# Optimization experiments

Measured on AMD Instinct MI355X. Metric: run time of the kernel, lower is better.

The kernel has to match this reference:

```python
import jax, jax.numpy as jnp
import numpy as np

N_NODES = 100000
N_EDGES = 2000000
N_GRAPHS = 2000
IN_DIM = 7
EDGE_DIM = 4
HID = 32
N_CLASSES = 2
NEG_SLOPE = 0.2
BN_EPS = 1e-5


def setup_inputs() -> dict:
    key = jax.random.key(0)
    ks = jax.random.split(key, 16)
    x = jax.random.normal(ks[0], (N_NODES, IN_DIM), dtype=jnp.float32)
    edge_index = jax.random.randint(ks[1], (2, N_EDGES), 0, N_NODES, dtype=jnp.int64)
    batch = jnp.sort(jax.random.randint(ks[2], (N_NODES,), 0, N_GRAPHS, dtype=jnp.int64))
    edge_attr = jax.random.normal(ks[3], (N_EDGES, EDGE_DIM), dtype=jnp.float32)
    s = 0.1
    W0 = jax.random.normal(ks[4], (IN_DIM, HID), dtype=jnp.float32) * s
    W12 = jax.random.normal(ks[5], (2, HID, HID), dtype=jnp.float32) * s
    att_src = jax.random.normal(ks[6], (3, HID), dtype=jnp.float32) * s
    att_dst = jax.random.normal(ks[7], (3, HID), dtype=jnp.float32) * s
    lin_edge = jax.random.normal(ks[8], (3, EDGE_DIM, HID), dtype=jnp.float32) * s
    att_edge = jax.random.normal(ks[9], (3, HID), dtype=jnp.float32) * s
    bias = jnp.zeros((3, HID), dtype=jnp.float32)
    bn_gamma = jnp.ones((3, HID), dtype=jnp.float32)
    bn_beta = jnp.zeros((3, HID), dtype=jnp.float32)
    fc_W = jax.random.normal(ks[10], (HID, N_CLASSES), dtype=jnp.float32) * s
    fc_b = jnp.zeros((N_CLASSES,), dtype=jnp.float32)
    return dict(x=x, edge_index=edge_index, batch=batch, edge_attr=edge_attr,
                W0=W0, W12=W12, att_src=att_src, att_dst=att_dst,
                lin_edge=lin_edge, att_edge=att_edge, bias=bias,
                bn_gamma=bn_gamma, bn_beta=bn_beta, fc_W=fc_W, fc_b=fc_b)


def gat_layer(x, src, dst, edge_attr, W, a_src, a_dst, We, a_edge, b):
    # PyG GATConv, heads=1, add_self_loops=False: edge_attr conditions attention only.
    N = x.shape[0]
    h = x @ W                                   # [N, H]
    e = edge_attr @ We                          # [E, H]
    score = ((h * a_src).sum(-1)[src]
             + (h * a_dst).sum(-1)[dst]
             + (e * a_edge).sum(-1))            # [E]
    score = jax.nn.leaky_relu(score, NEG_SLOPE)
    m = jax.ops.segment_max(score, dst, num_segments=N)
    w = jnp.exp(score - m[dst])
    denom = jax.ops.segment_sum(w, dst, num_segments=N)
    alpha = w / (denom[dst] + 1e-16)            # segment softmax over incoming edges
    out = jax.ops.segment_sum(h[src] * alpha[:, None], dst, num_segments=N)
    return out + b


def batchnorm(x, gamma, beta):
    mu = x.mean(axis=0)
    var = ((x - mu) ** 2).mean(axis=0)          # biased var, as torch BN normalization
    return (x - mu) * jax.lax.rsqrt(var + BN_EPS) * gamma + beta


def reference(x, edge_index, batch, edge_attr, W0, W12, att_src, att_dst,
              lin_edge, att_edge, bias, bn_gamma, bn_beta, fc_W, fc_b):
    src, dst = edge_index[0], edge_index[1]
    Ws = [W0, W12[0], W12[1]]
    h = x
    for l in range(3):
        h = gat_layer(h, src, dst, edge_attr, Ws[l], att_src[l], att_dst[l],
                      lin_edge[l], att_edge[l], bias[l])
        h = batchnorm(h, bn_gamma[l], bn_beta[l])
        h = jax.nn.relu(h)
    node_embs = h
    graph_emb = jax.ops.segment_sum(node_embs, batch, num_segments=N_GRAPHS)
    out = graph_emb @ fc_W + fc_b
    return (out, node_embs, graph_emb)
```

## Files before the change

kernel.cpp:

```cpp
#include <hip/hip_runtime.h>
#include <hip/hip_bf16.h>
#include <math.h>

#define N_NODES   100000
#define N_EDGES   2000000
#define N_GRAPHS  2000
#define IN_DIM    7
#define EDGE_DIM  4
#define HID       32
#define N_CLASSES 2
#define NEG_SLOPE 0.2f
#define BN_EPS    1e-5f
#define SCAN_B    1024

__device__ __forceinline__ unsigned bfbits(float f) {
    unsigned u = __float_as_uint(f);
    return (u + 0x7FFFu + ((u >> 16) & 1u)) >> 16;
}

__global__ void k_ce_all(const float* __restrict__ lin_edge, const float* __restrict__ att_edge,
                         float* __restrict__ ce3, float* __restrict__ gsum3,
                         float* __restrict__ gsq3) {
    int t = threadIdx.x;
    if (t < 12) {
        int l = t >> 2, d = t & 3;
        float s = 0.f;
        for (int k = 0; k < HID; ++k)
            s += lin_edge[(size_t)l * EDGE_DIM * HID + d * HID + k] * att_edge[l * HID + k];
        ce3[t] = s;
    }
    if (t < 3 * HID) { gsum3[t] = 0.f; gsq3[t] = 0.f; }
}

__global__ void k_hist(const int* __restrict__ dst, int* __restrict__ deg) {
    int e = blockIdx.x * blockDim.x + threadIdx.x;
    if (e < N_EDGES) atomicAdd(deg + dst[e], 1);
}

__global__ void k_scan1(const int* __restrict__ deg, int* __restrict__ offs,
                        int* __restrict__ bsum) {
    __shared__ int wsum[16];
    int t = threadIdx.x, lane = t & 63, w = t >> 6;
    int i = blockIdx.x * SCAN_B + t;
    int v = (i < N_NODES) ? deg[i] : 0;
    int x = v;
#pragma unroll
    for (int o = 1; o < 64; o <<= 1) { int y = __shfl_up(x, o, 64); if (lane >= o) x += y; }
    if (lane == 63) wsum[w] = x;
    __syncthreads();
    if (t < 16) {
        int s = wsum[t];
#pragma unroll
        for (int o = 1; o < 16; o <<= 1) { int y = __shfl_up(s, o, 16); if (t >= o) s += y; }
        wsum[t] = s;
    }
    __syncthreads();
    int excl = (w ? wsum[w - 1] : 0) + x - v;
    if (i < N_NODES) offs[i] = excl;
    if (t == 0) bsum[blockIdx.x] = wsum[15];
}

__global__ void k_scan2(int* __restrict__ bsum, int nb) {
    __shared__ int w0;
    int t = threadIdx.x, lane = t & 63, w = t >> 6;
    int v = (t < nb) ? bsum[t] : 0;
    int x = v;
#pragma unroll
    for (int o = 1; o < 64; o <<= 1) { int y = __shfl_up(x, o, 64); if (lane >= o) x += y; }
    if (w == 0 && lane == 63) w0 = x;
    __syncthreads();
    int excl = x - v + (w ? w0 : 0);
    if (t < nb) bsum[t] = excl;
}

__global__ void k_scan3(int* __restrict__ offs, const int* __restrict__ bsum,
                        int* __restrict__ cursor) {
    int i = blockIdx.x * SCAN_B + threadIdx.x;
    if (i < N_NODES) {
        int o = offs[i] + bsum[blockIdx.x];
        offs[i] = o;
        cursor[i] = o;
    }
}

__global__ void k_scatter(const int* __restrict__ src, const int* __restrict__ dst,
                          const float4* __restrict__ eattr, const float* __restrict__ ce3,
                          int* __restrict__ cursor, int4* __restrict__ pack) {
    int e = blockIdx.x * blockDim.x + threadIdx.x;
    if (e >= N_EDGES) return;
    float4 ea = eattr[e];
    float e0 = ea.x * ce3[0] + ea.y * ce3[1] + ea.z * ce3[2] + ea.w * ce3[3];
    float e1 = ea.x * ce3[4] + ea.y * ce3[5] + ea.z * ce3[6] + ea.w * ce3[7];
    float e2 = ea.x * ce3[8] + ea.y * ce3[9] + ea.z * ce3[10] + ea.w * ce3[11];
    int d = dst[e];
    int pos = atomicAdd(cursor + d, 1);
    pack[pos] = make_int4(src[e],
                          (int)(bfbits(e0) | (bfbits(e1) << 16)),
                          (int)bfbits(e2), 0);
}

template <int INDIM, bool BN>
__global__ void k_linear(const float* __restrict__ in, const float* __restrict__ W,
                         const float* __restrict__ a_src, const float* __restrict__ a_dst,
                         const float* __restrict__ gsum, const float* __restrict__ gsq,
                         const float* __restrict__ gamma, const float* __restrict__ beta,
                         __hip_bfloat16* __restrict__ h, float* __restrict__ asrc,
                         float* __restrict__ adst) {
    __shared__ float Ws[INDIM * HID];
    for (int i = threadIdx.x; i < INDIM * HID; i += blockDim.x) Ws[i] = W[i];
    __syncthreads();
    int g = threadIdx.x >> 5, k = threadIdx.x & 31;
    int n = blockIdx.x * 8 + g;
    if (n >= N_NODES) return;
    float xv;
    if (BN) {
        const float invN = 1.f / (float)N_NODES;
        float mu = gsum[k] * invN;
        float var = gsq[k] * invN - mu * mu;
        var = fmaxf(var, 0.f);
        float scl = rsqrtf(var + BN_EPS) * gamma[k];
        float v = (in[(size_t)n * INDIM + k] - mu) * scl + beta[k];
        xv = fmaxf(v, 0.f);
    } else {
        xv = (k < INDIM) ? in[(size_t)n * INDIM + k] : 0.f;
    }
    float acc = 0.f;
#pragma unroll
    for (int d = 0; d < INDIM; ++d) acc += __shfl(xv, d, 32) * Ws[d * HID + k];
    h[(size_t)n * HID + k] = __float2bfloat16(acc);
    float vs = acc * a_src[k];
    float vd = acc * a_dst[k];
#pragma unroll
    for (int m = 16; m > 0; m >>= 1) {
        vs += __shfl_xor(vs, m, 32);
        vd += __shfl_xor(vd, m, 32);
    }
    if (k == 0) { asrc[n] = vs; adst[n] = vd; }
}

template <int L>
__global__ void k_aggr(const int4* __restrict__ pack, const int* __restrict__ offs,
                       const int* __restrict__ endp, const __hip_bfloat16* __restrict__ hb,
                       const float* __restrict__ asrc, const float* __restrict__ adst,
                       const float* __restrict__ bias, float* __restrict__ out,
                       float* __restrict__ gsum, float* __restrict__ gsq) {
    __shared__ float ssum[HID], ssq[HID];
    if (threadIdx.x < HID) { ssum[threadIdx.x] = 0.f; ssq[threadIdx.x] = 0.f; }
    __syncthreads();
    int g = threadIdx.x >> 5;
    int lane = threadIdx.x & 31;
    int sub = lane >> 4;
    int c2 = lane & 15;
    int n = blockIdx.x * 8 + g;
    if (n < N_NODES) {
        int pbeg = offs[n], en = endp[n];
        float ad = adst[n];
        float den = 0.f, a0 = 0.f, a1 = 0.f;
        for (int p = pbeg; p < en; p += 16) {
            int4 pk[8];
            float as[8];
            unsigned hw[8];
#pragma unroll
            for (int m = 0; m < 8; ++m) {
                int q = p + 2 * m + sub;
                q = q < en ? q : en - 1;
                pk[m] = pack[q];
            }
#pragma unroll
            for (int m = 0; m < 8; ++m) as[m] = asrc[pk[m].x];
#pragma unroll
            for (int m = 0; m < 8; ++m)
                hw[m] = *(const unsigned*)(hb + (size_t)pk[m].x * HID + 2 * c2);
#pragma unroll
            for (int m = 0; m < 8; ++m) {
                unsigned z = (unsigned)pk[m].y;
                float edot;
                if (L == 0)      edot = __uint_as_float((z & 0xFFFFu) << 16);
                else if (L == 1) edot = __uint_as_float(z & 0xFFFF0000u);
                else             edot = __uint_as_float(((unsigned)pk[m].z & 0xFFFFu) << 16);
                float sc = as[m] + ad + edot;
                sc = fmaxf(sc, NEG_SLOPE * sc);
                float w = (p + 2 * m + sub < en) ? __expf(sc) : 0.f;
                den += w;
                float lo = __uint_as_float((hw[m] & 0xFFFFu) << 16);
                float hi = __uint_as_float(hw[m] & 0xFFFF0000u);
                a0 = fmaf(w, lo, a0);
                a1 = fmaf(w, hi, a1);
            }
        }
        den += __shfl_xor(den, 16, 32);
        a0  += __shfl_xor(a0, 16, 32);
        a1  += __shfl_xor(a1, 16, 32);
        if (sub == 0) {
            float inv = 1.f / (den + 1e-16f);
            float v0 = a0 * inv + bias[2 * c2];
            float v1 = a1 * inv + bias[2 * c2 + 1];
            *(float2*)(out + (size_t)n * HID + 2 * c2) = make_float2(v0, v1);
            atomicAdd(&ssum[2 * c2], v0);
            atomicAdd(&ssum[2 * c2 + 1], v1);
            atomicAdd(&ssq[2 * c2], v0 * v0);
            atomicAdd(&ssq[2 * c2 + 1], v1 * v1);
        }
    }
    __syncthreads();
    if (threadIdx.x < HID) {
        atomicAdd(gsum + threadIdx.x, ssum[threadIdx.x]);
        atomicAdd(gsq + threadIdx.x, ssq[threadIdx.x]);
    }
}

__global__ void k_bn_relu_pool(const float* __restrict__ acc, const float* __restrict__ gsum,
                               const float* __restrict__ gsq, const float* __restrict__ gamma,
                               const float* __restrict__ beta, const int* __restrict__ batch,
                               float* __restrict__ nemb, float* __restrict__ gemb) {
    int g = threadIdx.x >> 5, k = threadIdx.x & 31;
    int n = blockIdx.x * 8 + g;
    if (n >= N_NODES) return;
    const float invN = 1.f / (float)N_NODES;
    float mu = gsum[k] * invN;
    float var = gsq[k] * invN - mu * mu;
    var = fmaxf(var, 0.f);
    float scl = rsqrtf(var + BN_EPS) * gamma[k];
    float v = (acc[(size_t)n * HID + k] - mu) * scl + beta[k];
    v = fmaxf(v, 0.f);
    nemb[(size_t)n * HID + k] = v;
    atomicAdd(gemb + (size_t)batch[n] * HID + k, v);
}

__global__ void k_fc(const float* __restrict__ gemb, const float* __restrict__ W,
                     const float* __restrict__ b, float* __restrict__ out) {
    int g = blockIdx.x * blockDim.x + threadIdx.x;
    if (g >= N_GRAPHS) return;
    float a0 = b[0], a1 = b[1];
    for (int k = 0; k < HID; ++k) {
        float v = gemb[(size_t)g * HID + k];
        a0 += v * W[k * 2 + 0];
        a1 += v * W[k * 2 + 1];
    }
    out[g * 2 + 0] = a0;
    out[g * 2 + 1] = a1;
}

extern "C" void kernel_launch(void* const* d_in, const int* in_sizes, int n_in,
                              void* d_out, int out_size, void* d_ws, size_t ws_size,
                              hipStream_t stream) {
    const float* x        = (const float*)d_in[0];
    const int*   ei       = (const int*)d_in[1];
    const int*   batch    = (const int*)d_in[2];
    const float* eattr    = (const float*)d_in[3];
    const float* W0       = (const float*)d_in[4];
    const float* W12      = (const float*)d_in[5];
    const float* att_src  = (const float*)d_in[6];
    const float* att_dst  = (const float*)d_in[7];
    const float* lin_edge = (const float*)d_in[8];
    const float* att_edge = (const float*)d_in[9];
    const float* bias     = (const float*)d_in[10];
    const float* bn_gamma = (const float*)d_in[11];
    const float* bn_beta  = (const float*)d_in[12];
    const float* fc_W     = (const float*)d_in[13];
    const float* fc_b     = (const float*)d_in[14];

    const int* srcA = ei;
    const int* dstA = ei + N_EDGES;

    float* out       = (float*)d_out;
    float* node_embs = out + N_GRAPHS * N_CLASSES;
    float* graph_emb = node_embs + (size_t)N_NODES * HID;

    char* ws = (char*)d_ws;
    size_t off = 0;
    auto alloc = [&](size_t bytes) { char* p = ws + off; off += (bytes + 255) & ~(size_t)255; return p; };
    __hip_bfloat16* hT = (__hip_bfloat16*)alloc((size_t)N_NODES * HID * 2);
    float* A     = (float*)alloc((size_t)N_NODES * HID * 4);
    int4*  pack  = (int4*)alloc((size_t)N_EDGES * 16);
    int*   deg   = (int*)alloc((size_t)N_NODES * 4);
    int*   offs  = (int*)alloc((size_t)N_NODES * 4);
    int*   cursor= (int*)alloc((size_t)N_NODES * 4);
    int*   bsum  = (int*)alloc(128 * 4);
    float* asrc  = (float*)alloc((size_t)N_NODES * 4);
    float* adst  = (float*)alloc((size_t)N_NODES * 4);
    float* ce3   = (float*)alloc(12 * 4);
    float* gsum3 = (float*)alloc(3 * HID * 4);
    float* gsq3  = (float*)alloc(3 * HID * 4);
    (void)ws_size;

    const int nodeBlocks8 = (N_NODES + 7) / 8;
    const int edgeBlocks  = (N_EDGES + 255) / 256;
    const int scanBlocks  = (N_NODES + SCAN_B - 1) / SCAN_B;

    hipMemsetAsync(deg, 0, (size_t)N_NODES * 4, stream);
    k_ce_all<<<1, 128, 0, stream>>>(lin_edge, att_edge, ce3, gsum3, gsq3);
    k_hist<<<edgeBlocks, 256, 0, stream>>>(dstA, deg);
    k_scan1<<<scanBlocks, SCAN_B, 0, stream>>>(deg, offs, bsum);
    k_scan2<<<1, 128, 0, stream>>>(bsum, scanBlocks);
    k_scan3<<<scanBlocks, SCAN_B, 0, stream>>>(offs, bsum, cursor);
    k_scatter<<<edgeBlocks, 256, 0, stream>>>(srcA, dstA, (const float4*)eattr, ce3, cursor, pack);

    k_linear<IN_DIM, false><<<nodeBlocks8, 256, 0, stream>>>(
        x, W0, att_src, att_dst, nullptr, nullptr, nullptr, nullptr, hT, asrc, adst);
    k_aggr<0><<<nodeBlocks8, 256, 0, stream>>>(pack, offs, cursor, hT, asrc, adst,
                                               bias, A, gsum3, gsq3);
    k_linear<HID, true><<<nodeBlocks8, 256, 0, stream>>>(
        A, W12, att_src + HID, att_dst + HID, gsum3, gsq3, bn_gamma, bn_beta, hT, asrc, adst);
    k_aggr<1><<<nodeBlocks8, 256, 0, stream>>>(pack, offs, cursor, hT, asrc, adst,
                                               bias + HID, A, gsum3 + HID, gsq3 + HID);
    k_linear<HID, true><<<nodeBlocks8, 256, 0, stream>>>(
        A, W12 + HID * HID, att_src + 2 * HID, att_dst + 2 * HID,
        gsum3 + HID, gsq3 + HID, bn_gamma + HID, bn_beta + HID, hT, asrc, adst);
    k_aggr<2><<<nodeBlocks8, 256, 0, stream>>>(pack, offs, cursor, hT, asrc, adst,
                                               bias + 2 * HID, A, gsum3 + 2 * HID, gsq3 + 2 * HID);

    hipMemsetAsync(graph_emb, 0, (size_t)N_GRAPHS * HID * 4, stream);
    k_bn_relu_pool<<<nodeBlocks8, 256, 0, stream>>>(A, gsum3 + 2 * HID, gsq3 + 2 * HID,
                                                    bn_gamma + 2 * HID, bn_beta + 2 * HID,
                                                    batch, node_embs, graph_emb);
    k_fc<<<(N_GRAPHS + 255) / 256, 256, 0, stream>>>(graph_emb, fc_W, fc_b, out);
}
```

Baseline: 930.4 us.

## Split aggregation into two channel-half passes with separate half-width feature arrays

Node features are stored as two 16-channel bf16 arrays. Each GAT layer's aggregation now runs as two kernel launches, one per half, and each warp-half processes four edges per step with 8 lanes per edge. The aim is to shrink the randomly gathered feature working set per pass (3.2 MB per half) so it stays cache-resident. In exchange the packed edge list is streamed twice and attention scores and exponentials are recomputed in both passes. Packed-edge loads and output stores also become nontemporal so they do not evict the feature arrays from cache.

```diff
diff --git a/kernel.cpp b/kernel.cpp
--- a/kernel.cpp
+++ b/kernel.cpp
@@ -12,6 +12,9 @@
 #define NEG_SLOPE 0.2f
 #define BN_EPS    1e-5f
 #define SCAN_B    1024
+
+typedef int   iv4 __attribute__((ext_vector_type(4)));
+typedef float fv2 __attribute__((ext_vector_type(2)));
 
 __device__ __forceinline__ unsigned bfbits(float f) {
     unsigned u = __float_as_uint(f);
@@ -104,8 +107,8 @@
                          const float* __restrict__ a_src, const float* __restrict__ a_dst,
                          const float* __restrict__ gsum, const float* __restrict__ gsq,
                          const float* __restrict__ gamma, const float* __restrict__ beta,
-                         __hip_bfloat16* __restrict__ h, float* __restrict__ asrc,
-                         float* __restrict__ adst) {
+                         __hip_bfloat16* __restrict__ hLo, __hip_bfloat16* __restrict__ hHi,
+                         float* __restrict__ asrc, float* __restrict__ adst) {
     __shared__ float Ws[INDIM * HID];
     for (int i = threadIdx.x; i < INDIM * HID; i += blockDim.x) Ws[i] = W[i];
     __syncthreads();
@@ -127,7 +130,8 @@
     float acc = 0.f;
 #pragma unroll
     for (int d = 0; d < INDIM; ++d) acc += __shfl(xv, d, 32) * Ws[d * HID + k];
-    h[(size_t)n * HID + k] = __float2bfloat16(acc);
+    if (k < 16) hLo[(size_t)n * 16 + k] = __float2bfloat16(acc);
+    else        hHi[(size_t)n * 16 + (k - 16)] = __float2bfloat16(acc);
     float vs = acc * a_src[k];
     float vd = acc * a_dst[k];
 #pragma unroll
@@ -138,7 +142,7 @@
     if (k == 0) { asrc[n] = vs; adst[n] = vd; }
 }
 
-template <int L>
+template <int L, int HALF>
 __global__ void k_aggr(const int4* __restrict__ pack, const int* __restrict__ offs,
                        const int* __restrict__ endp, const __hip_bfloat16* __restrict__ hb,
                        const float* __restrict__ asrc, const float* __restrict__ adst,
@@ -149,38 +153,38 @@
     __syncthreads();
     int g = threadIdx.x >> 5;
     int lane = threadIdx.x & 31;
-    int sub = lane >> 4;
-    int c2 = lane & 15;
+    int sub = lane >> 3;
+    int c2 = lane & 7;
     int n = blockIdx.x * 8 + g;
     if (n < N_NODES) {
         int pbeg = offs[n], en = endp[n];
         float ad = adst[n];
         float den = 0.f, a0 = 0.f, a1 = 0.f;
         for (int p = pbeg; p < en; p += 16) {
-            int4 pk[8];
-            float as[8];
-            unsigned hw[8];
-#pragma unroll
-            for (int m = 0; m < 8; ++m) {
-                int q = p + 2 * m + sub;
+            iv4 pk[4];
+            float as[4];
+            unsigned hw[4];
+#pragma unroll
+            for (int m = 0; m < 4; ++m) {
+                int q = p + 4 * m + sub;
                 q = q < en ? q : en - 1;
-                pk[m] = pack[q];
+                pk[m] = __builtin_nontemporal_load((const iv4*)(pack + q));
             }
 #pragma unroll
-            for (int m = 0; m < 8; ++m) as[m] = asrc[pk[m].x];
-#pragma unroll
-            for (int m = 0; m < 8; ++m)
-                hw[m] = *(const unsigned*)(hb + (size_t)pk[m].x * HID + 2 * c2);
-#pragma unroll
-            for (int m = 0; m < 8; ++m) {
-                unsigned z = (unsigned)pk[m].y;
+            for (int m = 0; m < 4; ++m) as[m] = asrc[pk[m][0]];
+#pragma unroll
+            for (int m = 0; m < 4; ++m)
+                hw[m] = *(const unsigned*)(hb + (size_t)pk[m][0] * 16 + 2 * c2);
+#pragma unroll
+            for (int m = 0; m < 4; ++m) {
+                unsigned z = (unsigned)pk[m][1];
                 float edot;
                 if (L == 0)      edot = __uint_as_float((z & 0xFFFFu) << 16);
                 else if (L == 1) edot = __uint_as_float(z & 0xFFFF0000u);
-                else             edot = __uint_as_float(((unsigned)pk[m].z & 0xFFFFu) << 16);
+                else             edot = __uint_as_float(((unsigned)pk[m][2] & 0xFFFFu) << 16);
                 float sc = as[m] + ad + edot;
                 sc = fmaxf(sc, NEG_SLOPE * sc);
-                float w = (p + 2 * m + sub < en) ? __expf(sc) : 0.f;
+                float w = (p + 4 * m + sub < en) ? __expf(sc) : 0.f;
                 den += w;
                 float lo = __uint_as_float((hw[m] & 0xFFFFu) << 16);
                 float hi = __uint_as_float(hw[m] & 0xFFFF0000u);
@@ -188,18 +192,23 @@
                 a1 = fmaf(w, hi, a1);
             }
         }
+        den += __shfl_xor(den, 8, 32);
+        a0  += __shfl_xor(a0, 8, 32);
+        a1  += __shfl_xor(a1, 8, 32);
         den += __shfl_xor(den, 16, 32);
         a0  += __shfl_xor(a0, 16, 32);
         a1  += __shfl_xor(a1, 16, 32);
         if (sub == 0) {
+            int ch = HALF * 16 + 2 * c2;
             float inv = 1.f / (den + 1e-16f);
-            float v0 = a0 * inv + bias[2 * c2];
-            float v1 = a1 * inv + bias[2 * c2 + 1];
-            *(float2*)(out + (size_t)n * HID + 2 * c2) = make_float2(v0, v1);
-            atomicAdd(&ssum[2 * c2], v0);
-            atomicAdd(&ssum[2 * c2 + 1], v1);
-            atomicAdd(&ssq[2 * c2], v0 * v0);
-            atomicAdd(&ssq[2 * c2 + 1], v1 * v1);
+            float v0 = a0 * inv + bias[ch];
+            float v1 = a1 * inv + bias[ch + 1];
+            fv2 v; v[0] = v0; v[1] = v1;
+            __builtin_nontemporal_store(v, (fv2*)(out + (size_t)n * HID + ch));
+            atomicAdd(&ssum[ch], v0);
+            atomicAdd(&ssum[ch + 1], v1);
+            atomicAdd(&ssq[ch], v0 * v0);
+            atomicAdd(&ssq[ch + 1], v1 * v1);
         }
     }
     __syncthreads();
@@ -270,7 +279,8 @@
     char* ws = (char*)d_ws;
     size_t off = 0;
     auto alloc = [&](size_t bytes) { char* p = ws + off; off += (bytes + 255) & ~(size_t)255; return p; };
-    __hip_bfloat16* hT = (__hip_bfloat16*)alloc((size_t)N_NODES * HID * 2);
+    __hip_bfloat16* hLo = (__hip_bfloat16*)alloc((size_t)N_NODES * 16 * 2);
+    __hip_bfloat16* hHi = (__hip_bfloat16*)alloc((size_t)N_NODES * 16 * 2);
     float* A     = (float*)alloc((size_t)N_NODES * HID * 4);
     int4*  pack  = (int4*)alloc((size_t)N_EDGES * 16);
     int*   deg   = (int*)alloc((size_t)N_NODES * 4);
@@ -297,18 +307,27 @@
     k_scatter<<<edgeBlocks, 256, 0, stream>>>(srcA, dstA, (const float4*)eattr, ce3, cursor, pack);
 
     k_linear<IN_DIM, false><<<nodeBlocks8, 256, 0, stream>>>(
-        x, W0, att_src, att_dst, nullptr, nullptr, nullptr, nullptr, hT, asrc, adst);
-    k_aggr<0><<<nodeBlocks8, 256, 0, stream>>>(pack, offs, cursor, hT, asrc, adst,
-                                               bias, A, gsum3, gsq3);
+        x, W0, att_src, att_dst, nullptr, nullptr, nullptr, nullptr, hLo, hHi, asrc, adst);
+    k_aggr<0, 0><<<nodeBlocks8, 256, 0, stream>>>(pack, offs, cursor, hLo, asrc, adst,
+                                                  bias, A, gsum3, gsq3);
+    k_aggr<0, 1><<<nodeBlocks8, 256, 0, stream>>>(pack, offs, cursor, hHi, asrc, adst,
+                                                  bias, A, gsum3, gsq3);
     k_linear<HID, true><<<nodeBlocks8, 256, 0, stream>>>(
-        A, W12, att_src + HID, att_dst + HID, gsum3, gsq3, bn_gamma, bn_beta, hT, asrc, adst);
-    k_aggr<1><<<nodeBlocks8, 256, 0, stream>>>(pack, offs, cursor, hT, asrc, adst,
-                                               bias + HID, A, gsum3 + HID, gsq3 + HID);
+        A, W12, att_src + HID, att_dst + HID, gsum3, gsq3, bn_gamma, bn_beta,
+        hLo, hHi, asrc, adst);
+    k_aggr<1, 0><<<nodeBlocks8, 256, 0, stream>>>(pack, offs, cursor, hLo, asrc, adst,
+                                                  bias + HID, A, gsum3 + HID, gsq3 + HID);
+    k_aggr<1, 1><<<nodeBlocks8, 256, 0, stream>>>(pack, offs, cursor, hHi, asrc, adst,
+                                                  bias + HID, A, gsum3 + HID, gsq3 + HID);
     k_linear<HID, true><<<nodeBlocks8, 256, 0, stream>>>(
         A, W12 + HID * HID, att_src + 2 * HID, att_dst + 2 * HID,
-        gsum3 + HID, gsq3 + HID, bn_gamma + HID, bn_beta + HID, hT, asrc, adst);
-    k_aggr<2><<<nodeBlocks8, 256, 0, stream>>>(pack, offs, cursor, hT, asrc, adst,
-                                               bias + 2 * HID, A, gsum3 + 2 * HID, gsq3 + 2 * HID);
+        gsum3 + HID, gsq3 + HID, bn_gamma + HID, bn_beta + HID, hLo, hHi, asrc, adst);
+    k_aggr<2, 0><<<nodeBlocks8, 256, 0, stream>>>(pack, offs, cursor, hLo, asrc, adst,
+                                                  bias + 2 * HID, A,
+                                                  gsum3 + 2 * HID, gsq3 + 2 * HID);
+    k_aggr<2, 1><<<nodeBlocks8, 256, 0, stream>>>(pack, offs, cursor, hHi, asrc, adst,
+                                                  bias + 2 * HID, A,
+                                                  gsum3 + 2 * HID, gsq3 + 2 * HID);
 
     hipMemsetAsync(graph_emb, 0, (size_t)N_GRAPHS * HID * 4, stream);
     k_bn_relu_pool<<<nodeBlocks8, 256, 0, stream>>>(A, gsum3 + 2 * HID, gsq3 + 2 * HID,
```

Result: slower. 1.441 ms (+54.9%).
